# Performance work log

Measured on AMD Instinct MI355X. Metric: run time of the kernel, lower is better.

The kernel has to match this reference:

```python
import jax, jax.numpy as jnp
import numpy as np

N = 100000   # total nodes across the ragged graph batch
E = 800000   # edges
B = 4096     # graphs
V = 103      # element vocab (embedding rows)
D_IN = 200   # embedding dim
H = 256      # hidden dim


def setup_inputs() -> dict:
    key = jax.random.key(0)
    ks = jax.random.split(key, 20)
    s = 0.05
    return {
        "weight": jax.random.normal(ks[0], (V, D_IN), jnp.float32),
        "sto_x": jax.random.randint(ks[1], (N,), 0, V),
        "sto_edge_index": jax.random.randint(ks[2], (2, E), 0, N),
        "sto_weight": jax.random.uniform(ks[3], (N,), jnp.float32),
        "sto_batch": jnp.sort(jax.random.randint(ks[4], (N,), 0, B)),
        "gW0": jax.random.normal(ks[5], (D_IN, H), jnp.float32) * s,
        "gb0": jnp.zeros((H,), jnp.float32),
        "gW1": jax.random.normal(ks[6], (H, H), jnp.float32) * s,
        "gb1": jnp.zeros((H,), jnp.float32),
        "gW2": jax.random.normal(ks[7], (H, H), jnp.float32) * s,
        "gb2": jnp.zeros((H,), jnp.float32),
        "lstm_Wih": jax.random.normal(ks[8], (4 * H, 2 * H), jnp.float32) * s,
        "lstm_Whh": jax.random.normal(ks[9], (4 * H, H), jnp.float32) * s,
        "lstm_bih": jnp.zeros((4 * H,), jnp.float32),
        "lstm_bhh": jnp.zeros((4 * H,), jnp.float32),
        "mlin_W": jax.random.normal(ks[10], (H, 2 * H), jnp.float32) * s,
        "mlin_b": jnp.zeros((H,), jnp.float32),
        "p0W": jax.random.normal(ks[11], (128, H), jnp.float32) * s,
        "p0b": jnp.zeros((128,), jnp.float32),
        "p1W": jax.random.normal(ks[12], (128, 128), jnp.float32) * s,
        "p1b": jnp.zeros((128,), jnp.float32),
        "p2W": jax.random.normal(ks[13], (1, 128), jnp.float32) * s,
        "p2b": jnp.zeros((1,), jnp.float32),
    }


def reference(weight, sto_x, sto_edge_index, sto_weight, sto_batch,
              gW0, gb0, gW1, gb1, gW2, gb2,
              lstm_Wih, lstm_Whh, lstm_bih, lstm_bhh,
              mlin_W, mlin_b, p0W, p0b, p1W, p1b, p2W, p2b):
    # embedding gather (sto_x - 1, with -1 wrapping to the last row as in torch)
    x = weight[sto_x - 1]

    # --- GCN (3 layers, symmetric norm with self-loops, ReLU between layers) ---
    loop = jnp.arange(N)
    src = jnp.concatenate([sto_edge_index[0], loop])
    dst = jnp.concatenate([sto_edge_index[1], loop])
    deg = jax.ops.segment_sum(jnp.ones_like(dst, jnp.float32), dst, N)
    dinv = jax.lax.rsqrt(jnp.maximum(deg, 1.0))
    norm = (dinv[src] * dinv[dst])[:, None]

    def conv(h_in, W, b):
        hw = h_in @ W                                   # [N, H]
        return jax.ops.segment_sum(hw[src] * norm, dst, N) + b

    x = jax.nn.relu(conv(x, gW0, gb0))
    x = jax.nn.relu(conv(x, gW1, gb1))
    x = conv(x, gW2, gb2)

    # --- stoichiometric weighting + graph-wise scatter sum ---
    wx = x * sto_weight[:, None]                        # [N, H]
    sto = jax.ops.segment_sum(wx, sto_batch, B)         # [B, H]

    # --- Set2Set pooling (2 processing steps, 1-layer LSTM) ---
    h = jnp.zeros((B, H), wx.dtype)
    c = jnp.zeros((B, H), wx.dtype)
    q_star = jnp.zeros((B, 2 * H), wx.dtype)
    for _ in range(2):
        gates = q_star @ lstm_Wih.T + lstm_bih + h @ lstm_Whh.T + lstm_bhh
        i, f, g, o = jnp.split(gates, 4, axis=-1)
        c = jax.nn.sigmoid(f) * c + jax.nn.sigmoid(i) * jnp.tanh(g)
        h = jax.nn.sigmoid(o) * jnp.tanh(c)
        e = jnp.sum(wx * h[sto_batch], axis=-1)         # [N]
        emax = jax.ops.segment_max(e, sto_batch, B)
        a = jnp.exp(e - emax[sto_batch])
        a = a / (jax.ops.segment_sum(a, sto_batch, B)[sto_batch] + 1e-16)
        r = jax.ops.segment_sum(wx * a[:, None], sto_batch, B)
        q_star = jnp.concatenate([h, r], axis=-1)

    mean = q_star @ mlin_W.T + mlin_b + sto
    mean = mean / jnp.maximum(jnp.linalg.norm(mean, axis=1, keepdims=True), 1e-12)

    # --- predictor MLP (LeakyReLU slope 0.01) ---
    y = jax.nn.leaky_relu(mean @ p0W.T + p0b)
    y = jax.nn.leaky_relu(y @ p1W.T + p1b)
    return y @ p2W.T + p2b                              # [B, 1]
```

## Files before the change

### kernel.cpp

```cpp
#include <hip/hip_runtime.h>
#include <math.h>

constexpr int Nn  = 100000;
constexpr int Ee  = 800000;
constexpr int Bb  = 4096;
constexpr int Vv  = 103;
constexpr int DIN = 200;
constexpr int Hh  = 256;
constexpr int KV  = 128;

constexpr int SCHUNK = 1024;
constexpr int NSCAN  = (Nn + SCHUNK - 1)/SCHUNK;

using short8 = __attribute__((ext_vector_type(8))) short;
using f32x4  = __attribute__((ext_vector_type(4))) float;

__device__ __forceinline__ float sigf(float x){ return 1.f/(1.f+expf(-x)); }

__device__ __forceinline__ unsigned short f2bf(float f){
  unsigned int u = __float_as_uint(f);
  u += 0x7FFFu + ((u >> 16) & 1u);
  return (unsigned short)(u >> 16);
}
__device__ __forceinline__ float bf2f(unsigned int u){
  return __uint_as_float((u & 0xFFFFu) << 16);
}

__global__ void k_transpose(const float* __restrict__ in, float* __restrict__ out, int R, int C){
  int idx = blockIdx.x*256 + threadIdx.x;
  if (idx >= R*C) return;
  int r = idx / C, c = idx % C;
  out[(size_t)c*R + r] = in[(size_t)r*C + c];
}

__global__ void k_transpose_b(const float* __restrict__ in, unsigned short* __restrict__ out, int R, int C){
  int idx = blockIdx.x*256 + threadIdx.x;
  if (idx >= R*C) return;
  int r = idx / C, c = idx % C;
  out[(size_t)c*R + r] = f2bf(in[(size_t)r*C + c]);
}

__global__ void k_castb(const float* __restrict__ in, unsigned short* __restrict__ out, int n){
  int i = blockIdx.x*256 + threadIdx.x;
  if (i < n) out[i] = f2bf(in[i]);
}

__global__ void k_wg0t(const float* __restrict__ WG0, unsigned short* __restrict__ WG0tb){
  int i = blockIdx.x*256 + threadIdx.x;
  if (i >= Hh*KV) return;
  int n = i >> 7, k = i & (KV-1);
  float v = (k < Vv) ? WG0[(size_t)k*Hh + n] : 0.f;
  WG0tb[i] = f2bf(v);
}

__global__ void k_packW(const float* __restrict__ Wih, const float* __restrict__ Whh,
                        unsigned short* __restrict__ Wp){
  int i = blockIdx.x*256 + threadIdx.x;
  if (i >= 4*Hh*3*Hh) return;
  int g = i / (3*Hh), j = i % (3*Hh);
  float v = (j < 2*Hh) ? Wih[(size_t)g*2*Hh + j] : Whh[(size_t)g*Hh + (j - 2*Hh)];
  Wp[i] = f2bf(v);
}

__global__ void k_count(const int* __restrict__ dst, int* __restrict__ counts){
  int e = blockIdx.x*256 + threadIdx.x;
  if (e < Ee) atomicAdd(&counts[dst[e]], 1);
}

__global__ void k_dinv(const int* __restrict__ counts, float* __restrict__ dinv){
  int n = blockIdx.x*256 + threadIdx.x;
  if (n < Nn) dinv[n] = rsqrtf((float)(counts[n] + 1));
}

__global__ void k_scan1(const int* __restrict__ counts, int* __restrict__ partial){
  __shared__ int red[256];
  int t = threadIdx.x;
  int base = blockIdx.x*SCHUNK + t*4;
  int s = 0;
  if (base + 3 < Nn){ int4 v = *reinterpret_cast<const int4*>(counts + base); s = v.x+v.y+v.z+v.w; }
  else { for (int i=0;i<4;++i) if (base+i<Nn) s += counts[base+i]; }
  red[t] = s; __syncthreads();
  for (int st=128; st>0; st>>=1){ if (t<st) red[t]+=red[t+st]; __syncthreads(); }
  if (t==0) partial[blockIdx.x] = red[0];
}

__global__ void k_scan2(int* __restrict__ partial, int n){
  __shared__ int buf[128];
  int t = threadIdx.x;
  int v = (t < n) ? partial[t] : 0;
  buf[t] = v; __syncthreads();
  for (int off=1; off<128; off<<=1){
    int tv = (t>=off) ? buf[t-off] : 0;
    __syncthreads();
    buf[t] += tv;
    __syncthreads();
  }
  if (t < n) partial[t] = buf[t] - v;
}

__global__ void k_scan3(const int* __restrict__ counts, const int* __restrict__ partial,
                        int* __restrict__ offs){
  __shared__ int red[256];
  int t = threadIdx.x;
  int base = blockIdx.x*SCHUNK + t*4;
  int c0=0,c1=0,c2=0,c3=0;
  if (base + 3 < Nn){ int4 v = *reinterpret_cast<const int4*>(counts + base); c0=v.x;c1=v.y;c2=v.z;c3=v.w; }
  else { if (base<Nn) c0=counts[base]; if (base+1<Nn) c1=counts[base+1];
         if (base+2<Nn) c2=counts[base+2]; if (base+3<Nn) c3=counts[base+3]; }
  int s = c0+c1+c2+c3;
  red[t] = s; __syncthreads();
  for (int off=1; off<256; off<<=1){
    int tv = (t>=off) ? red[t-off] : 0;
    __syncthreads();
    red[t] += tv;
    __syncthreads();
  }
  int run = partial[blockIdx.x] + red[t] - s;
  if (base   < Nn) offs[base]   = run; run += c0;
  if (base+1 < Nn) offs[base+1] = run; run += c1;
  if (base+2 < Nn) offs[base+2] = run; run += c2;
  if (base+3 < Nn) offs[base+3] = run; run += c3;
  if (blockIdx.x == gridDim.x-1 && t == 255) offs[Nn] = partial[blockIdx.x] + red[255];
}

__global__ void k_copyi(const int* __restrict__ a, int* __restrict__ b, int n){
  int i = blockIdx.x*256 + threadIdx.x;
  if (i < n) b[i] = a[i];
}

__global__ void k_fill(const int* __restrict__ ei, const float* __restrict__ dinv,
                       int* __restrict__ fptr, uint2* __restrict__ epack){
  int e = blockIdx.x*256 + threadIdx.x;
  if (e >= Ee) return;
  int s = ei[e], d = ei[Ee + e];
  int pos = atomicAdd(&fptr[d], 1);
  epack[pos] = make_uint2((unsigned int)s, __float_as_uint(dinv[s]*dinv[d]));
}

__global__ void k_boffs(const int* __restrict__ batch, int* __restrict__ boffs){
  int b = blockIdx.x*256 + threadIdx.x;
  if (b > Bb) return;
  int lo = 0, hi = Nn;
  while (lo < hi){ int mid = (lo+hi)>>1; if (batch[mid] < b) lo = mid+1; else hi = mid; }
  boffs[b] = lo;
}

__global__ void k_hist(const int* __restrict__ sto_x, const int* __restrict__ offs,
                       const uint2* __restrict__ epack, const float* __restrict__ dinv,
                       unsigned short* __restrict__ Vb){
  __shared__ float hist[4][KV];
  int wid = threadIdx.x >> 6, lane = threadIdx.x & 63;
  int n = blockIdx.x*4 + wid;
  hist[wid][lane] = 0.f; hist[wid][lane+64] = 0.f;
  __syncthreads();
  int s = offs[n], e = offs[n+1];
  for (int k = s + lane; k < e; k += 64){
    uint2 ev = epack[k];
    int r2 = sto_x[ev.x]; r2 = (r2 == 0) ? (Vv-1) : r2-1;
    atomicAdd(&hist[wid][r2], __uint_as_float(ev.y));
  }
  if (lane == 0){
    int r0 = sto_x[n]; r0 = (r0 == 0) ? (Vv-1) : r0-1;
    float dn = dinv[n];
    atomicAdd(&hist[wid][r0], dn*dn);
  }
  __syncthreads();
  unsigned int p = ((unsigned int)f2bf(hist[wid][2*lane+1]) << 16) | f2bf(hist[wid][2*lane]);
  ((unsigned int*)Vb)[(size_t)n*(KV/2) + lane] = p;
}

__global__ void k_agg(const unsigned short* __restrict__ Xb, const int* __restrict__ offs,
                      const uint2* __restrict__ epack, const float* __restrict__ dinv,
                      unsigned short* __restrict__ T){
  int wid = threadIdx.x >> 6, lane = threadIdx.x & 63;
  int n = blockIdx.x*4 + wid;
  const uint2* Xv = (const uint2*)Xb;
  uint2 v = Xv[(size_t)n*64 + lane];
  float dn = dinv[n]; float s2 = dn*dn;
  float a0 = bf2f(v.x)*s2, a1 = bf2f(v.x>>16)*s2;
  float a2 = bf2f(v.y)*s2, a3 = bf2f(v.y>>16)*s2;
  int s = offs[n], e = offs[n+1];
  int k = s;
  for (; k + 7 < e; k += 8){
    uint2 ev[8], g[8];
    #pragma unroll
    for (int j = 0; j < 8; ++j) ev[j] = epack[k+j];
    #pragma unroll
    for (int j = 0; j < 8; ++j) g[j] = Xv[(size_t)ev[j].x*64 + lane];
    #pragma unroll
    for (int j = 0; j < 8; ++j){
      float nn = __uint_as_float(ev[j].y);
      a0 += bf2f(g[j].x)*nn; a1 += bf2f(g[j].x>>16)*nn;
      a2 += bf2f(g[j].y)*nn; a3 += bf2f(g[j].y>>16)*nn;
    }
  }
  for (; k + 1 < e; k += 2){
    uint2 e0 = epack[k], e1 = epack[k+1];
    uint2 g0 = Xv[(size_t)e0.x*64 + lane];
    uint2 g1 = Xv[(size_t)e1.x*64 + lane];
    float n0 = __uint_as_float(e0.y), n1 = __uint_as_float(e1.y);
    a0 += bf2f(g0.x)*n0; a1 += bf2f(g0.x>>16)*n0; a2 += bf2f(g0.y)*n0; a3 += bf2f(g0.y>>16)*n0;
    a0 += bf2f(g1.x)*n1; a1 += bf2f(g1.x>>16)*n1; a2 += bf2f(g1.y)*n1; a3 += bf2f(g1.y>>16)*n1;
  }
  if (k < e){
    uint2 e0 = epack[k];
    uint2 g0 = Xv[(size_t)e0.x*64 + lane];
    float n0 = __uint_as_float(e0.y);
    a0 += bf2f(g0.x)*n0; a1 += bf2f(g0.x>>16)*n0;
    a2 += bf2f(g0.y)*n0; a3 += bf2f(g0.y>>16)*n0;
  }
  uint2 o;
  o.x = (unsigned int)f2bf(a0) | ((unsigned int)f2bf(a1) << 16);
  o.y = (unsigned int)f2bf(a2) | ((unsigned int)f2bf(a3) << 16);
  ((uint2*)T)[(size_t)n*64 + lane] = o;
}

__global__ __launch_bounds__(512) void k_gemm8(
    const unsigned short* __restrict__ A, int lda,
    const unsigned short* __restrict__ Bt,
    const float* __restrict__ bias, const float* __restrict__ rowscale,
    const float* __restrict__ addf,
    float* __restrict__ Cf, unsigned short* __restrict__ Cb,
    int M, int K, int Nc, int relu)
{
  __shared__ unsigned short lds[18432];
  unsigned short (*Al)[40] = (unsigned short(*)[40])lds;
  unsigned short (*Bl)[40] = (unsigned short(*)[40])(lds + 128*40);

  int tid = threadIdx.x;
  int w = tid >> 6, lane = tid & 63;
  int wr = (w >> 1)*32, wc = (w & 1)*64;
  int l16 = lane & 15, kh = lane >> 4;
  int rbase = blockIdx.y*128, cbase = blockIdx.x*128;
  int sr = tid >> 2, sb = tid & 3;

  f32x4 acc[2][4] = {};

  for (int k0 = 0; k0 < K; k0 += 32){
    int kk = k0 + sb*8;
    uint4 a0 = make_uint4(0,0,0,0);
    int ar0 = rbase + sr;
    if (ar0 < M) a0 = *reinterpret_cast<const uint4*>(A + (size_t)ar0*lda + kk);
    uint4 b0 = *reinterpret_cast<const uint4*>(Bt + (size_t)(cbase + sr)*K + kk);
    __syncthreads();
    *reinterpret_cast<uint4*>(&Al[sr][sb*8]) = a0;
    *reinterpret_cast<uint4*>(&Bl[sr][sb*8]) = b0;
    __syncthreads();

    short8 af[2], bfv[4];
    #pragma unroll
    for (int m = 0; m < 2; ++m) af[m] = *reinterpret_cast<const short8*>(&Al[wr + m*16 + l16][kh*8]);
    #pragma unroll
    for (int n2 = 0; n2 < 4; ++n2) bfv[n2] = *reinterpret_cast<const short8*>(&Bl[wc + n2*16 + l16][kh*8]);
    #pragma unroll
    for (int m = 0; m < 2; ++m)
      #pragma unroll
      for (int n2 = 0; n2 < 4; ++n2)
        acc[m][n2] = __builtin_amdgcn_mfma_f32_16x16x32_bf16(af[m], bfv[n2], acc[m][n2], 0, 0, 0);
  }

  if (Cf){
    #pragma unroll
    for (int n2 = 0; n2 < 4; ++n2){
      int col = cbase + wc + n2*16 + l16;
      float bv = bias ? bias[col] : 0.f;
      #pragma unroll
      for (int m = 0; m < 2; ++m){
        #pragma unroll
        for (int i = 0; i < 4; ++i){
          int row = rbase + wr + m*16 + kh*4 + i;
          if (row >= M) continue;
          float v = acc[m][n2][i] + bv;
          if (addf) v += addf[(size_t)row*Nc + col];
          if (rowscale) v *= rowscale[row];
          if (relu == 1) v = fmaxf(v, 0.f);
          else if (relu == 2) v = (v > 0.f) ? v : 0.01f*v;
          Cf[(size_t)row*Nc + col] = v;
        }
      }
    }
  }
  if (Cb){
    __syncthreads();
    unsigned short* eps = lds + w*(32*72);
    #pragma unroll
    for (int n2 = 0; n2 < 4; ++n2){
      int colg = cbase + wc + n2*16 + l16;
      float bv = bias ? bias[colg] : 0.f;
      #pragma unroll
      for (int m = 0; m < 2; ++m){
        #pragma unroll
        for (int i = 0; i < 4; ++i){
          int lrow = m*16 + kh*4 + i;
          int rowg = rbase + wr + lrow;
          float v = acc[m][n2][i] + bv;
          float rs = (rowscale && rowg < M) ? rowscale[rowg] : 1.f;
          v *= rs;
          if (relu == 1) v = fmaxf(v, 0.f);
          else if (relu == 2) v = (v > 0.f) ? v : 0.01f*v;
          eps[lrow*72 + n2*16 + l16] = f2bf(v);
        }
      }
    }
    int c8 = lane & 7;
    #pragma unroll
    for (int rd = 0; rd < 4; ++rd){
      int lrow = rd*8 + (lane >> 3);
      int rowg = rbase + wr + lrow;
      short8 vv = *reinterpret_cast<const short8*>(&eps[lrow*72 + c8*8]);
      if (rowg < M)
        *reinterpret_cast<short8*>(Cb + (size_t)rowg*Nc + cbase + wc + c8*8) = vv;
    }
  }
}

__global__ __launch_bounds__(256) void k_gemm_nt(
    const float* __restrict__ A, const float* __restrict__ Bt,
    const float* __restrict__ bias, const float* __restrict__ Dadd,
    float* __restrict__ C, int M, int K, int Nc, int accum, int act)
{
  __shared__ float As[64][20];
  __shared__ float Bs[64][20];
  int tid = threadIdx.x;
  int rbase = blockIdx.y*64, cbase = blockIdx.x*64;
  int ty = tid>>4, tx = tid&15;
  int lr = tid>>2, lq = tid&3;
  float acc[4][4] = {};
  for (int k0 = 0; k0 < K; k0 += 16){
    float4 av = make_float4(0,0,0,0), bv = make_float4(0,0,0,0);
    int kk = k0 + lq*4;
    int ar = rbase + lr;
    if (ar < M && kk < K){
      if (kk + 3 < K) av = *reinterpret_cast<const float4*>(A + (size_t)ar*K + kk);
      else { float t0[4] = {0,0,0,0}; for (int i=0; i<4 && kk+i<K; ++i) t0[i] = A[(size_t)ar*K + kk + i];
             av = make_float4(t0[0],t0[1],t0[2],t0[3]); }
    }
    int br = cbase + lr;
    if (br < Nc && kk < K){
      if (kk + 3 < K) bv = *reinterpret_cast<const float4*>(Bt + (size_t)br*K + kk);
      else { float t0[4] = {0,0,0,0}; for (int i=0; i<4 && kk+i<K; ++i) t0[i] = Bt[(size_t)br*K + kk + i];
             bv = make_float4(t0[0],t0[1],t0[2],t0[3]); }
    }
    __syncthreads();
    *reinterpret_cast<float4*>(&As[lr][lq*4]) = av;
    *reinterpret_cast<float4*>(&Bs[lr][lq*4]) = bv;
    __syncthreads();
    #pragma unroll
    for (int kc = 0; kc < 16; kc += 4){
      float4 a4[4], b4[4];
      #pragma unroll
      for (int i=0;i<4;++i) a4[i] = *reinterpret_cast<float4*>(&As[ty*4+i][kc]);
      #pragma unroll
      for (int j=0;j<4;++j) b4[j] = *reinterpret_cast<float4*>(&Bs[tx*4+j][kc]);
      #pragma unroll
      for (int i=0;i<4;++i)
        #pragma unroll
        for (int j=0;j<4;++j)
          acc[i][j] += a4[i].x*b4[j].x + a4[i].y*b4[j].y + a4[i].z*b4[j].z + a4[i].w*b4[j].w;
    }
  }
  #pragma unroll
  for (int i=0;i<4;++i){
    int r = rbase + ty*4 + i;
    if (r >= M) continue;
    #pragma unroll
    for (int j=0;j<4;++j){
      int cc = cbase + tx*4 + j;
      if (cc >= Nc) continue;
      float v = acc[i][j];
      if (accum) v += C[(size_t)r*Nc + cc];
      if (bias)  v += bias[cc];
      if (Dadd)  v += Dadd[(size_t)r*Nc + cc];
      if (act == 1) v = (v > 0.f) ? v : 0.01f*v;
      C[(size_t)r*Nc + cc] = v;
    }
  }
}

__global__ void k_bsum(const float* __restrict__ bih, const float* __restrict__ bhh,
                       float* __restrict__ bsum){
  int g = blockIdx.x*256 + threadIdx.x;
  if (g < 4*Hh) bsum[g] = bih[g] + bhh[g];
}

__global__ void k_lstm(const float* __restrict__ gates, float* __restrict__ cbuf,
                       float* __restrict__ hbuf, unsigned short* __restrict__ qh){
  int idx = blockIdx.x*256 + threadIdx.x;
  if (idx >= Bb*Hh) return;
  int b = idx >> 8, ch = idx & 255;
  const float* g = gates + (size_t)b*4*Hh;
  float ig = sigf(g[ch]);
  float fg = sigf(g[Hh + ch]);
  float gg = tanhf(g[2*Hh + ch]);
  float og = sigf(g[3*Hh + ch]);
  float cn = fg*cbuf[idx] + ig*gg;
  float hn = og*tanhf(cn);
  cbuf[idx] = cn; hbuf[idx] = hn;
  unsigned short hb = f2bf(hn);
  qh[(size_t)b*3*Hh + ch] = hb;
  qh[(size_t)b*3*Hh + 2*Hh + ch] = hb;
}

__global__ void k_pool(const unsigned short* __restrict__ wxb,
                       const float* __restrict__ hbuf,
                       const int* __restrict__ boffs,
                       unsigned short* __restrict__ qh,
                       float* __restrict__ sto, int do_sto){
  int wid = threadIdx.x >> 6, lane = threadIdx.x & 63;
  int g = blockIdx.x*4 + wid;
  if (g >= Bb) return;
  const uint2* Xv = (const uint2*)wxb;
  float4 hv = ((const float4*)hbuf)[(size_t)g*64 + lane];
  int s = boffs[g], e = boffs[g+1];
  float m = -INFINITY, ssum = 0.f;
  float a0=0.f,a1=0.f,a2=0.f,a3=0.f;
  float t0=0.f,t1=0.f,t2=0.f,t3=0.f;
  for (int n = s; n < e; ++n){
    uint2 v = Xv[(size_t)n*64 + lane];
    float x0=bf2f(v.x), x1=bf2f(v.x>>16), x2=bf2f(v.y), x3=bf2f(v.y>>16);
    if (do_sto){ t0+=x0; t1+=x1; t2+=x2; t3+=x3; }
    float d = x0*hv.x + x1*hv.y + x2*hv.z + x3*hv.w;
    #pragma unroll
    for (int mask=32; mask; mask>>=1) d += __shfl_xor(d, mask, 64);
    if (d > m){
      float sc = expf(m - d);
      ssum = ssum*sc + 1.f;
      a0 = a0*sc + x0; a1 = a1*sc + x1; a2 = a2*sc + x2; a3 = a3*sc + x3;
      m = d;
    } else {
      float p = expf(d - m);
      ssum += p;
      a0 += p*x0; a1 += p*x1; a2 += p*x2; a3 += p*x3;
    }
  }
  float inv = 1.f/(ssum + 1e-16f);
  uint2 o;
  o.x = (unsigned int)f2bf(a0*inv) | ((unsigned int)f2bf(a1*inv) << 16);
  o.y = (unsigned int)f2bf(a2*inv) | ((unsigned int)f2bf(a3*inv) << 16);
  ((uint2*)(qh + (size_t)g*3*Hh + Hh))[lane] = o;
  if (do_sto) ((float4*)sto)[(size_t)g*64 + lane] = make_float4(t0,t1,t2,t3);
}

__global__ void k_norm(float* __restrict__ mean, unsigned short* __restrict__ outb){
  __shared__ float red[256];
  int b = blockIdx.x, tid = threadIdx.x;
  float v = mean[(size_t)b*Hh + tid];
  red[tid] = v*v; __syncthreads();
  for (int st=128; st>0; st>>=1){ if (tid<st) red[tid] += red[tid+st]; __syncthreads(); }
  float nrm = fmaxf(sqrtf(red[0]), 1e-12f);
  float o = v/nrm;
  outb[(size_t)b*Hh + tid] = f2bf(o);
}

__global__ void k_out(const float* __restrict__ y1, const float* __restrict__ p2W,
                      const float* __restrict__ p2b, float* __restrict__ out){
  __shared__ float red[128];
  int b = blockIdx.x, tid = threadIdx.x;
  float v = y1[(size_t)b*128 + tid]*p2W[tid];
  red[tid] = v; __syncthreads();
  for (int st=64; st>0; st>>=1){ if (tid<st) red[tid] += red[tid+st]; __syncthreads(); }
  if (tid == 0) out[b] = red[0] + p2b[0];
}

extern "C" void kernel_launch(void* const* d_in, const int* in_sizes, int n_in,
                              void* d_out, int out_size, void* d_ws, size_t ws_size,
                              hipStream_t stream) {
  const float* weight   = (const float*)d_in[0];
  const int*   sto_x    = (const int*)  d_in[1];
  const int*   ei       = (const int*)  d_in[2];
  const float* sto_w    = (const float*)d_in[3];
  const int*   batch    = (const int*)  d_in[4];
  const float* gW0 = (const float*)d_in[5];   const float* gb0 = (const float*)d_in[6];
  const float* gW1 = (const float*)d_in[7];   const float* gb1 = (const float*)d_in[8];
  const float* gW2 = (const float*)d_in[9];   const float* gb2 = (const float*)d_in[10];
  const float* Wih = (const float*)d_in[11];  const float* Whh = (const float*)d_in[12];
  const float* bih = (const float*)d_in[13];  const float* bhh = (const float*)d_in[14];
  const float* mW  = (const float*)d_in[15];  const float* mb  = (const float*)d_in[16];
  const float* p0W = (const float*)d_in[17];  const float* p0b = (const float*)d_in[18];
  const float* p1W = (const float*)d_in[19];  const float* p1b = (const float*)d_in[20];
  const float* p2W = (const float*)d_in[21];  const float* p2b = (const float*)d_in[22];
  float* out = (float*)d_out;

  char* w = (char*)d_ws;
  auto alloc = [&](size_t bytes)->char*{ char* p = w; w += (bytes + 255) & ~size_t(255); return p; };
  unsigned short* Xb = (unsigned short*)alloc((size_t)Nn*Hh*2);
  unsigned short* Tb = (unsigned short*)alloc((size_t)Nn*Hh*2);
  unsigned short* Vb = (unsigned short*)alloc((size_t)Nn*KV*2);
  float* WG0   = (float*)alloc((size_t)Vv*Hh*4);
  unsigned short* WG0tb = (unsigned short*)alloc((size_t)Hh*KV*2);
  float* gW0t  = (float*)alloc((size_t)Hh*DIN*4);
  unsigned short* gW1tb = (unsigned short*)alloc((size_t)Hh*Hh*2);
  unsigned short* gW2tb = (unsigned short*)alloc((size_t)Hh*Hh*2);
  unsigned short* Wpb   = (unsigned short*)alloc((size_t)4*Hh*3*Hh*2);
  unsigned short* mWb   = (unsigned short*)alloc((size_t)Hh*2*Hh*2);
  unsigned short* p0Wb  = (unsigned short*)alloc((size_t)128*Hh*2);
  unsigned short* p1Wb  = (unsigned short*)alloc((size_t)128*128*2);
  int*   counts= (int*)  alloc((size_t)Nn*4);
  int*   offs  = (int*)  alloc((size_t)(Nn+1)*4);
  int*   fptr  = (int*)  alloc((size_t)Nn*4);
  int*   spart = (int*)  alloc((size_t)NSCAN*4);
  float* dinv  = (float*)alloc((size_t)Nn*4);
  uint2* epack = (uint2*)alloc((size_t)Ee*8);
  int*   boffs = (int*)  alloc((size_t)(Bb+1)*4);
  float* sto   = (float*)alloc((size_t)Bb*Hh*4);
  float* hbuf  = (float*)alloc((size_t)Bb*Hh*4);
  float* cbuf  = (float*)alloc((size_t)Bb*Hh*4);
  unsigned short* qh = (unsigned short*)alloc((size_t)Bb*3*Hh*2);
  float* gates = (float*)alloc((size_t)Bb*4*Hh*4);
  float* bsum  = (float*)alloc((size_t)4*Hh*4);
  float* meanb = (float*)alloc((size_t)Bb*Hh*4);
  unsigned short* meanbb = (unsigned short*)alloc((size_t)Bb*Hh*2);
  unsigned short* y0b = (unsigned short*)alloc((size_t)Bb*128*2);
  float* y1    = (float*)alloc((size_t)Bb*128*4);

  auto gemm = [&](const float* A, const float* Bt, const float* bias, const float* Dadd,
                  float* C, int M, int K, int Nc, int accum, int act){
    dim3 g((Nc+63)/64, (M+63)/64);
    k_gemm_nt<<<g, 256, 0, stream>>>(A, Bt, bias, Dadd, C, M, K, Nc, accum, act);
  };
  auto gemm8 = [&](const unsigned short* A, int lda, const unsigned short* Bt,
                   const float* bias, const float* rowscale, const float* addf,
                   float* Cf, unsigned short* Cb, int M, int K, int Nc, int relu){
    dim3 g(Nc/128, (M+127)/128);
    k_gemm8<<<g, 512, 0, stream>>>(A, lda, Bt, bias, rowscale, addf, Cf, Cb, M, K, Nc, relu);
  };

  hipMemsetAsync(counts, 0, (size_t)Nn*4, stream);
  hipMemsetAsync(cbuf,  0, (size_t)Bb*Hh*4, stream);
  hipMemsetAsync(qh,    0, (size_t)Bb*3*Hh*2, stream);

  k_transpose<<<(DIN*Hh+255)/256, 256, 0, stream>>>(gW0, gW0t, DIN, Hh);
  k_transpose_b<<<(Hh*Hh+255)/256, 256, 0, stream>>>(gW1, gW1tb, Hh, Hh);
  k_transpose_b<<<(Hh*Hh+255)/256, 256, 0, stream>>>(gW2, gW2tb, Hh, Hh);
  k_packW<<<(4*Hh*3*Hh+255)/256, 256, 0, stream>>>(Wih, Whh, Wpb);
  k_castb<<<(Hh*2*Hh+255)/256, 256, 0, stream>>>(mW, mWb, Hh*2*Hh);
  k_castb<<<(128*Hh+255)/256, 256, 0, stream>>>(p0W, p0Wb, 128*Hh);
  k_castb<<<(128*128+255)/256, 256, 0, stream>>>(p1W, p1Wb, 128*128);

  k_count<<<(Ee+255)/256, 256, 0, stream>>>(ei + Ee, counts);
  k_dinv<<<(Nn+255)/256, 256, 0, stream>>>(counts, dinv);
  k_scan1<<<NSCAN, 256, 0, stream>>>(counts, spart);
  k_scan2<<<1, 128, 0, stream>>>(spart, NSCAN);
  k_scan3<<<NSCAN, 256, 0, stream>>>(counts, spart, offs);
  k_copyi<<<(Nn+255)/256, 256, 0, stream>>>(offs, fptr, Nn);
  k_fill<<<(Ee+255)/256, 256, 0, stream>>>(ei, dinv, fptr, epack);
  k_boffs<<<(Bb+256)/256, 256, 0, stream>>>(batch, boffs);

  gemm(weight, gW0t, nullptr, nullptr, WG0, Vv, DIN, Hh, 0, 0);
  k_wg0t<<<(Hh*KV+255)/256, 256, 0, stream>>>(WG0, WG0tb);
  k_hist<<<Nn/4, 256, 0, stream>>>(sto_x, offs, epack, dinv, Vb);
  gemm8(Vb, KV, WG0tb, gb0, nullptr, nullptr, nullptr, Xb, Nn, KV, Hh, 1);

  k_agg<<<Nn/4, 256, 0, stream>>>(Xb, offs, epack, dinv, Tb);
  gemm8(Tb, Hh, gW1tb, gb1, nullptr, nullptr, nullptr, Xb, Nn, Hh, Hh, 1);
  k_agg<<<Nn/4, 256, 0, stream>>>(Xb, offs, epack, dinv, Tb);
  gemm8(Tb, Hh, gW2tb, gb2, sto_w, nullptr, nullptr, Xb, Nn, Hh, Hh, 0);

  k_bsum<<<(4*Hh+255)/256, 256, 0, stream>>>(bih, bhh, bsum);

  for (int t = 0; t < 2; ++t){
    gemm8(qh, 3*Hh, Wpb, bsum, nullptr, nullptr, gates, nullptr, Bb, 3*Hh, 4*Hh, 0);
    k_lstm<<<(Bb*Hh+255)/256, 256, 0, stream>>>(gates, cbuf, hbuf, qh);
    k_pool<<<Bb/4, 256, 0, stream>>>(Xb, hbuf, boffs, qh, sto, t == 0);
  }

  gemm8(qh, 3*Hh, mWb, mb, nullptr, sto, meanb, nullptr, Bb, 2*Hh, Hh, 0);
  k_norm<<<Bb, Hh, 0, stream>>>(meanb, meanbb);
  gemm8(meanbb, Hh, p0Wb, p0b, nullptr, nullptr, nullptr, y0b, Bb, Hh, 128, 2);
  gemm8(y0b, 128, p1Wb, p1b, nullptr, nullptr, y1, nullptr, Bb, 128, 128, 2);
  k_out<<<Bb, 128, 0, stream>>>(y1, p2W, p2b, out);
}
```

Baseline: 567.8 us.

## Add 64x256-tile bf16 MFMA GEMM with K=64 steps and use it for node GEMMs

Adds a new GEMM kernel that tiles 64 rows by 256 columns with a 64-wide K step. Each block covers the full hidden width, so the A tile is loaded once per row block instead of being reloaded for each 128-column tile, and it halves the number of K-loop barriers. The bf16 epilogue is staged through LDS for 16-byte coalesced stores. The kernel replaces the older GEMM for the three GCN layers, the LSTM gates and the merge linear, in exchange for more LDS per block and possibly lower occupancy.

```diff
diff --git a/kernel.cpp b/kernel.cpp
--- a/kernel.cpp
+++ b/kernel.cpp
@@ -213,6 +213,116 @@
   o.x = (unsigned int)f2bf(a0) | ((unsigned int)f2bf(a1) << 16);
   o.y = (unsigned int)f2bf(a2) | ((unsigned int)f2bf(a3) << 16);
   ((uint2*)T)[(size_t)n*64 + lane] = o;
+}
+
+__global__ __launch_bounds__(512) void k_gemm64(
+    const unsigned short* __restrict__ A, int lda,
+    const unsigned short* __restrict__ Bt,
+    const float* __restrict__ bias, const float* __restrict__ rowscale,
+    const float* __restrict__ addf,
+    float* __restrict__ Cf, unsigned short* __restrict__ Cb,
+    int M, int K, int Nc, int relu)
+{
+  __shared__ unsigned short lds[23040];
+  unsigned short (*Al)[72] = (unsigned short(*)[72])lds;
+  unsigned short (*Bl)[72] = (unsigned short(*)[72])(lds + 64*72);
+
+  int tid = threadIdx.x;
+  int w = tid >> 6, lane = tid & 63;
+  int wr = (w >> 2)*32, wc = (w & 3)*64;
+  int l16 = lane & 15, kh = lane >> 4;
+  int rbase = blockIdx.y*64, cbase = blockIdx.x*256;
+  int sr = tid >> 3, sb = tid & 7;
+
+  f32x4 acc[2][4] = {};
+
+  for (int k0 = 0; k0 < K; k0 += 64){
+    int kk = k0 + sb*8;
+    uint4 a0 = make_uint4(0,0,0,0);
+    int ar = rbase + sr;
+    if (ar < M) a0 = *reinterpret_cast<const uint4*>(A + (size_t)ar*lda + kk);
+    uint4 b0 = *reinterpret_cast<const uint4*>(Bt + (size_t)(cbase + sr      )*K + kk);
+    uint4 b1 = *reinterpret_cast<const uint4*>(Bt + (size_t)(cbase + sr +  64)*K + kk);
+    uint4 b2 = *reinterpret_cast<const uint4*>(Bt + (size_t)(cbase + sr + 128)*K + kk);
+    uint4 b3 = *reinterpret_cast<const uint4*>(Bt + (size_t)(cbase + sr + 192)*K + kk);
+    __syncthreads();
+    *reinterpret_cast<uint4*>(&Al[sr][sb*8])     = a0;
+    *reinterpret_cast<uint4*>(&Bl[sr][sb*8])     = b0;
+    *reinterpret_cast<uint4*>(&Bl[sr+64][sb*8])  = b1;
+    *reinterpret_cast<uint4*>(&Bl[sr+128][sb*8]) = b2;
+    *reinterpret_cast<uint4*>(&Bl[sr+192][sb*8]) = b3;
+    __syncthreads();
+
+    #pragma unroll
+    for (int kq = 0; kq < 2; ++kq){
+      short8 af[2], bfv[4];
+      #pragma unroll
+      for (int m = 0; m < 2; ++m)
+        af[m] = *reinterpret_cast<const short8*>(&Al[wr + m*16 + l16][kq*32 + kh*8]);
+      #pragma unroll
+      for (int n2 = 0; n2 < 4; ++n2)
+        bfv[n2] = *reinterpret_cast<const short8*>(&Bl[wc + n2*16 + l16][kq*32 + kh*8]);
+      #pragma unroll
+      for (int m = 0; m < 2; ++m)
+        #pragma unroll
+        for (int n2 = 0; n2 < 4; ++n2)
+          acc[m][n2] = __builtin_amdgcn_mfma_f32_16x16x32_bf16(af[m], bfv[n2], acc[m][n2], 0, 0, 0);
+    }
+  }
+
+  if (Cf){
+    #pragma unroll
+    for (int n2 = 0; n2 < 4; ++n2){
+      int col = cbase + wc + n2*16 + l16;
+      float bv = bias ? bias[col] : 0.f;
+      #pragma unroll
+      for (int m = 0; m < 2; ++m){
+        #pragma unroll
+        for (int i = 0; i < 4; ++i){
+          int row = rbase + wr + m*16 + kh*4 + i;
+          if (row >= M) continue;
+          float v = acc[m][n2][i] + bv;
+          if (addf) v += addf[(size_t)row*Nc + col];
+          if (rowscale) v *= rowscale[row];
+          if (relu == 1) v = fmaxf(v, 0.f);
+          else if (relu == 2) v = (v > 0.f) ? v : 0.01f*v;
+          Cf[(size_t)row*Nc + col] = v;
+        }
+      }
+    }
+  }
+  if (Cb){
+    __syncthreads();
+    unsigned short* eps = lds + w*(32*72);
+    #pragma unroll
+    for (int n2 = 0; n2 < 4; ++n2){
+      int colg = cbase + wc + n2*16 + l16;
+      float bv = bias ? bias[colg] : 0.f;
+      #pragma unroll
+      for (int m = 0; m < 2; ++m){
+        #pragma unroll
+        for (int i = 0; i < 4; ++i){
+          int lrow = m*16 + kh*4 + i;
+          int rowg = rbase + wr + lrow;
+          float v = acc[m][n2][i] + bv;
+          float rs = (rowscale && rowg < M) ? rowscale[rowg] : 1.f;
+          v *= rs;
+          if (relu == 1) v = fmaxf(v, 0.f);
+          else if (relu == 2) v = (v > 0.f) ? v : 0.01f*v;
+          eps[lrow*72 + n2*16 + l16] = f2bf(v);
+        }
+      }
+    }
+    int c8 = lane & 7;
+    #pragma unroll
+    for (int rd = 0; rd < 4; ++rd){
+      int lrow = rd*8 + (lane >> 3);
+      int rowg = rbase + wr + lrow;
+      short8 vv = *reinterpret_cast<const short8*>(&eps[lrow*72 + c8*8]);
+      if (rowg < M)
+        *reinterpret_cast<short8*>(Cb + (size_t)rowg*Nc + cbase + wc + c8*8) = vv;
+    }
+  }
 }
 
 __global__ __launch_bounds__(512) void k_gemm8(
@@ -524,6 +634,12 @@
     dim3 g(Nc/128, (M+127)/128);
     k_gemm8<<<g, 512, 0, stream>>>(A, lda, Bt, bias, rowscale, addf, Cf, Cb, M, K, Nc, relu);
   };
+  auto gemm64 = [&](const unsigned short* A, int lda, const unsigned short* Bt,
+                    const float* bias, const float* rowscale, const float* addf,
+                    float* Cf, unsigned short* Cb, int M, int K, int Nc, int relu){
+    dim3 g(Nc/256, (M+63)/64);
+    k_gemm64<<<g, 512, 0, stream>>>(A, lda, Bt, bias, rowscale, addf, Cf, Cb, M, K, Nc, relu);
+  };
 
   hipMemsetAsync(counts, 0, (size_t)Nn*4, stream);
   hipMemsetAsync(cbuf,  0, (size_t)Bb*Hh*4, stream);
@@ -549,22 +665,22 @@
   gemm(weight, gW0t, nullptr, nullptr, WG0, Vv, DIN, Hh, 0, 0);
   k_wg0t<<<(Hh*KV+255)/256, 256, 0, stream>>>(WG0, WG0tb);
   k_hist<<<Nn/4, 256, 0, stream>>>(sto_x, offs, epack, dinv, Vb);
-  gemm8(Vb, KV, WG0tb, gb0, nullptr, nullptr, nullptr, Xb, Nn, KV, Hh, 1);
+  gemm64(Vb, KV, WG0tb, gb0, nullptr, nullptr, nullptr, Xb, Nn, KV, Hh, 1);
 
   k_agg<<<Nn/4, 256, 0, stream>>>(Xb, offs, epack, dinv, Tb);
-  gemm8(Tb, Hh, gW1tb, gb1, nullptr, nullptr, nullptr, Xb, Nn, Hh, Hh, 1);
+  gemm64(Tb, Hh, gW1tb, gb1, nullptr, nullptr, nullptr, Xb, Nn, Hh, Hh, 1);
   k_agg<<<Nn/4, 256, 0, stream>>>(Xb, offs, epack, dinv, Tb);
-  gemm8(Tb, Hh, gW2tb, gb2, sto_w, nullptr, nullptr, Xb, Nn, Hh, Hh, 0);
+  gemm64(Tb, Hh, gW2tb, gb2, sto_w, nullptr, nullptr, Xb, Nn, Hh, Hh, 0);
 
   k_bsum<<<(4*Hh+255)/256, 256, 0, stream>>>(bih, bhh, bsum);
 
   for (int t = 0; t < 2; ++t){
-    gemm8(qh, 3*Hh, Wpb, bsum, nullptr, nullptr, gates, nullptr, Bb, 3*Hh, 4*Hh, 0);
+    gemm64(qh, 3*Hh, Wpb, bsum, nullptr, nullptr, gates, nullptr, Bb, 3*Hh, 4*Hh, 0);
     k_lstm<<<(Bb*Hh+255)/256, 256, 0, stream>>>(gates, cbuf, hbuf, qh);
     k_pool<<<Bb/4, 256, 0, stream>>>(Xb, hbuf, boffs, qh, sto, t == 0);
   }
 
-  gemm8(qh, 3*Hh, mWb, mb, nullptr, sto, meanb, nullptr, Bb, 2*Hh, Hh, 0);
+  gemm64(qh, 3*Hh, mWb, mb, nullptr, sto, meanb, nullptr, Bb, 2*Hh, Hh, 0);
   k_norm<<<Bb, Hh, 0, stream>>>(meanb, meanbb);
   gemm8(meanbb, Hh, p0Wb, p0b, nullptr, nullptr, nullptr, y0b, Bb, Hh, 128, 2);
   gemm8(y0b, 128, p1Wb, p1b, nullptr, nullptr, y1, nullptr, Bb, 128, 128, 2);
```

Measured after the change: 560.3 us. No clear change (-1.3%).
